# Kernel tuning notes

Measured on AMD Instinct MI355X. Metric: run time of the kernel, lower is better.

## Reference

```python
import jax, jax.numpy as jnp
import numpy as np

M, NQ, NKV = 8, 256, 4096
E, H, D = 1024, 16, 64  # embed_dim, num_heads, head_dim
SCALE = D ** -0.5


def setup_inputs() -> dict:
    key = jax.random.key(0)
    ks = jax.random.split(key, 6)
    zq = jax.random.normal(ks[0], (M, NQ, E), dtype=jnp.float32)
    zkv = jax.random.normal(ks[1], (M, NKV, E), dtype=jnp.float32)
    xq = jax.random.normal(ks[2], (M, NQ, E), dtype=jnp.float32)
    xkv = jax.random.normal(ks[3], (M, NKV, E), dtype=jnp.float32)
    Wq = jax.random.normal(ks[4], (E, H * D), dtype=jnp.float32) / np.sqrt(E)
    Wk = jax.random.normal(ks[5], (E, H * D), dtype=jnp.float32) / np.sqrt(E)
    raw_head_weights = jnp.ones((H,), dtype=jnp.float32)
    return {"zq": zq, "zkv": zkv, "xq": xq, "xkv": xkv,
            "Wq": Wq, "Wk": Wk, "raw_head_weights": raw_head_weights}


def reference(zq, zkv, xq, xkv, Wq, Wk, raw_head_weights):
    # project + split heads: [m, h, n, d]
    q = jnp.einsum('mne,ehd->mhnd', zq, Wq.reshape(E, H, D))
    k = jnp.einsum('mne,ehd->mhnd', zkv, Wk.reshape(E, H, D))
    # SDPA with V = xkv broadcast across heads
    scores = jnp.einsum('mhqd,mhkd->mhqk', q, k) * SCALE
    attn = jax.nn.softmax(scores, axis=-1)
    # attn @ V with broadcast V [m, nkv, dx] -> per-head outputs [m, h, nq, dx]
    out = jnp.einsum('mhqk,mkd->mhqd', attn, xkv)
    # head-weighted combine + residual
    head_weights = jax.nn.softmax(raw_head_weights, axis=0)
    xq_update = jnp.einsum('mhqd,h->mqd', out, head_weights)
    xq_out = xq + xq_update
    return (zq, xq_out)
```

## Files before the change

### kernel.cpp

```cpp
#include <hip/hip_runtime.h>
#include <hip/hip_bf16.h>
#include <stdint.h>

#define MB_  8
#define NQ_  256
#define NKV_ 4096
#define E_   1024
#define H_   16
#define D_   64

typedef __bf16 bf16x8 __attribute__((ext_vector_type(8)));
typedef float  f32x4  __attribute__((ext_vector_type(4)));
typedef unsigned short u16;
typedef unsigned short u16x8 __attribute__((ext_vector_type(8)));

#define MFMA16(a,b,c) __builtin_amdgcn_mfma_f32_16x16x32_bf16((a),(b),(c),0,0,0)

__device__ __forceinline__ u16 f2bf(float f) {
  uint32_t u = __float_as_uint(f);
  u += 0x7fffu + ((u >> 16) & 1u);
  return (u16)(u >> 16);
}

__device__ __forceinline__ void gload_lds16(const void* g, void* l) {
  __builtin_amdgcn_global_load_lds(
      (const __attribute__((address_space(1))) void*)g,
      (__attribute__((address_space(3))) void*)l, 16, 0, 0);
}

__device__ __forceinline__ void stage_tile(const char* __restrict__ g, int ldbytes,
                                           char* lds, int t) {
  int srcCB = (((t & 7) ^ ((t >> 3) & 7)) << 4);
  const char* gp = g + (long long)(t >> 3) * ldbytes + srcCB;
  char* lp = lds + ((t >> 6) << 10);
#pragma unroll
  for (int i = 0; i < 4; ++i) {
    gload_lds16(gp + (long long)(32 * i) * ldbytes, lp + i * 4096);
  }
}

__device__ __forceinline__ bf16x8 read_frag(const char* lds, int r, int cb) {
  return *(const bf16x8*)(lds + r * 128 + (cb ^ ((r & 7) << 4)));
}

template <int MODE>
__global__ __launch_bounds__(256, 2) void gemm_nt(
    const u16* __restrict__ A, const u16* __restrict__ Bt, void* __restrict__ Cv,
    int lda, int ldb, int ldc, int K,
    long long sA, long long sB, long long sC) {
  __shared__ __align__(16) char smA[16384];
  __shared__ __align__(16) char smB[16384];
  int zz = blockIdx.z;
  int b = (MODE == 2) ? (zz & 7) : zz;
  int ks = (MODE == 2) ? (zz >> 3) : 0;
  long long koff = (long long)ks * 1024;

  unsigned nwg = gridDim.x * gridDim.y;
  unsigned orig = blockIdx.y * gridDim.x + blockIdx.x;
  unsigned cpx = nwg >> 3;
  unsigned swz = (orig & 7) * cpx + (orig >> 3);
  unsigned bx = swz % gridDim.x, by = swz / gridDim.x;

  const char* Ap = (const char*)(A + (long long)b * sA + (long long)by * 128 * lda + koff);
  const char* Bp = (const char*)(Bt + (long long)b * sB + (long long)bx * 128 * ldb + koff);

  int t = threadIdx.x, lane = t & 63;
  int wm = t >> 7, wn = (t >> 6) & 1;
  int rl = lane & 15, kq = lane >> 4;

  f32x4 acc[4][4];
#pragma unroll
  for (int i = 0; i < 4; ++i)
#pragma unroll
    for (int j = 0; j < 4; ++j) acc[i][j] = (f32x4){0.f, 0.f, 0.f, 0.f};

  int ldab = lda * 2, ldbb = ldb * 2;
  for (int k0 = 0; k0 < K; k0 += 64) {
    stage_tile(Ap + k0 * 2, ldab, smA, t);
    stage_tile(Bp + k0 * 2, ldbb, smB, t);
    __syncthreads();
    bf16x8 af[4][2], bf[4][2];
#pragma unroll
    for (int f = 0; f < 4; ++f)
#pragma unroll
      for (int ksl = 0; ksl < 2; ++ksl) {
        af[f][ksl] = read_frag(smA, wm * 64 + f * 16 + rl, ksl * 64 + kq * 16);
        bf[f][ksl] = read_frag(smB, wn * 64 + f * 16 + rl, ksl * 64 + kq * 16);
      }
#pragma unroll
    for (int fm = 0; fm < 4; ++fm)
#pragma unroll
      for (int fn = 0; fn < 4; ++fn) {
        acc[fm][fn] = MFMA16(af[fm][0], bf[fn][0], acc[fm][fn]);
        acc[fm][fn] = MFMA16(af[fm][1], bf[fn][1], acc[fm][fn]);
      }
    __syncthreads();
  }

#pragma unroll
  for (int fm = 0; fm < 4; ++fm)
#pragma unroll
    for (int fn = 0; fn < 4; ++fn)
#pragma unroll
      for (int j = 0; j < 4; ++j) {
        int row = by * 128 + wm * 64 + fm * 16 + kq * 4 + j;
        int col = bx * 128 + wn * 64 + fn * 16 + rl;
        if (MODE == 0) {
          ((u16*)Cv)[(long long)b * sC + (long long)row * ldc + col] = f2bf(acc[fm][fn][j]);
        } else {
          ((float*)Cv)[((long long)(ks * 8 + b)) * sC + (long long)row * ldc + col] =
              acc[fm][fn][j];
        }
      }
}

__global__ void pv_combine_copy(const float* __restrict__ part, const float* __restrict__ xq,
                                const float* __restrict__ zq, float* __restrict__ out0,
                                float* __restrict__ out1) {
  int bid = blockIdx.x;
  if (bid < 2048) {
    int i = bid * 256 + threadIdx.x;
    ((float4*)out0)[i] = ((const float4*)zq)[i];
  } else {
    int i = (bid - 2048) * 256 + threadIdx.x;
    float4 s = ((const float4*)xq)[i];
#pragma unroll
    for (int k = 0; k < 4; ++k) {
      float4 p = ((const float4*)(part + (long long)k * 2097152))[i];
      s.x += p.x; s.y += p.y; s.z += p.z; s.w += p.w;
    }
    ((float4*)out1)[i] = s;
  }
}

__global__ __launch_bounds__(256, 4) void attn_stats(
    const u16* __restrict__ qg, const u16* __restrict__ kg,
    float* __restrict__ lstP) {
  __shared__ __align__(16) char smQ[16384];
  __shared__ __align__(16) char smK[16384];
  int kt = blockIdx.x, qt = blockIdx.y;
  int m = blockIdx.z >> 1, hh = blockIdx.z & 1;
  int t = threadIdx.x, lane = t & 63;
  int wm = t >> 7, wn = (t >> 6) & 1;
  int rl = lane & 15, kq = lane >> 4;

  const char* qbase = (const char*)(qg + ((long long)(m * NQ_ + qt * 128)) * 1024);
  const char* kbase = (const char*)(kg + ((long long)(m * NKV_ + kt * 128)) * 1024);

  for (int hi = 0; hi < 8; ++hi) {
    int h = hh * 8 + hi;
    stage_tile(qbase + h * 128, 2048, smQ, t);
    stage_tile(kbase + h * 128, 2048, smK, t);
    __syncthreads();
    bf16x8 kf[4][2], qf[4][2];
#pragma unroll
    for (int f = 0; f < 4; ++f)
#pragma unroll
      for (int ksl = 0; ksl < 2; ++ksl) {
        kf[f][ksl] = read_frag(smK, wm * 64 + f * 16 + rl, ksl * 64 + kq * 16);
        qf[f][ksl] = read_frag(smQ, wn * 64 + f * 16 + rl, ksl * 64 + kq * 16);
      }
    float rs[4] = {0.f, 0.f, 0.f, 0.f};
#pragma unroll
    for (int fm = 0; fm < 4; ++fm)
#pragma unroll
      for (int fn = 0; fn < 4; ++fn) {
        f32x4 sc = (f32x4){0.f, 0.f, 0.f, 0.f};
        sc = MFMA16(kf[fm][0], qf[fn][0], sc);
        sc = MFMA16(kf[fm][1], qf[fn][1], sc);
        rs[fn] += (__expf(sc[0]) + __expf(sc[1])) + (__expf(sc[2]) + __expf(sc[3]));
      }
#pragma unroll
    for (int fn = 0; fn < 4; ++fn) {
      float v = rs[fn];
      v += __shfl_xor(v, 16);
      v += __shfl_xor(v, 32);
      if (lane < 16) {
        int q = qt * 128 + wn * 64 + fn * 16 + rl;
        lstP[(long long)(kt * 2 + wm) * 32768 + ((m * H_ + h) << 8) + q] = v;
      }
    }
    __syncthreads();
  }
}

__global__ void stats_combine(const float* __restrict__ lp, float* __restrict__ lst) {
  int i = blockIdx.x * 256 + threadIdx.x;
  float s = 0.f;
#pragma unroll
  for (int k = 0; k < 64; ++k) s += lp[(long long)k * 32768 + i];
  lst[i] = s;
}

__global__ __launch_bounds__(256, 2) void pbar_kernel(
    const u16* __restrict__ qg, const u16* __restrict__ kg,
    const float* __restrict__ lstat,
    const float* __restrict__ rawhw, u16* __restrict__ Pbar) {
  __shared__ __align__(16) char smQ[16384];
  __shared__ __align__(16) char smK[16384];
  __shared__ float scf[2048];
  int kt = blockIdx.x, qt = blockIdx.y, m = blockIdx.z;
  int q0 = qt * 128, k0 = kt * 128;
  int t = threadIdx.x, lane = t & 63;
  int wm = t >> 7, wn = (t >> 6) & 1;
  int rl = lane & 15, kq = lane >> 4;

  float hm = -1e30f;
  for (int i = 0; i < H_; ++i) hm = fmaxf(hm, rawhw[i]);
  float hs = 0.f, hw[H_];
  for (int i = 0; i < H_; ++i) { hw[i] = __expf(rawhw[i] - hm); hs += hw[i]; }
  float hinv = 1.f / hs;
  for (int idx = t; idx < 2048; idx += 256) {
    int h = idx >> 7, r = idx & 127;
    scf[idx] = hw[h] * hinv / lstat[((m * H_ + h) << 8) + q0 + r];
  }

  f32x4 pacc[4][4];
#pragma unroll
  for (int i = 0; i < 4; ++i)
#pragma unroll
    for (int j = 0; j < 4; ++j) pacc[i][j] = (f32x4){0.f, 0.f, 0.f, 0.f};

  const char* qbase = (const char*)(qg + ((long long)(m * NQ_ + q0)) * 1024);
  const char* kbase = (const char*)(kg + ((long long)(m * NKV_ + k0)) * 1024);

  for (int h = 0; h < H_; ++h) {
    stage_tile(qbase + h * 128, 2048, smQ, t);
    stage_tile(kbase + h * 128, 2048, smK, t);
    __syncthreads();
    bf16x8 af[4][2], bfr[4][2];
#pragma unroll
    for (int f = 0; f < 4; ++f)
#pragma unroll
      for (int ksl = 0; ksl < 2; ++ksl) {
        af[f][ksl] = read_frag(smQ, wm * 64 + f * 16 + rl, ksl * 64 + kq * 16);
        bfr[f][ksl] = read_frag(smK, wn * 64 + f * 16 + rl, ksl * 64 + kq * 16);
      }
#pragma unroll
    for (int fm = 0; fm < 4; ++fm) {
      int rbase = wm * 64 + fm * 16 + kq * 4;
      float cf0 = scf[(h << 7) + rbase + 0];
      float cf1 = scf[(h << 7) + rbase + 1];
      float cf2 = scf[(h << 7) + rbase + 2];
      float cf3 = scf[(h << 7) + rbase + 3];
#pragma unroll
      for (int fn = 0; fn < 4; ++fn) {
        f32x4 sc = (f32x4){0.f, 0.f, 0.f, 0.f};
        sc = MFMA16(af[fm][0], bfr[fn][0], sc);
        sc = MFMA16(af[fm][1], bfr[fn][1], sc);
        pacc[fm][fn][0] += cf0 * __expf(sc[0]);
        pacc[fm][fn][1] += cf1 * __expf(sc[1]);
        pacc[fm][fn][2] += cf2 * __expf(sc[2]);
        pacc[fm][fn][3] += cf3 * __expf(sc[3]);
      }
    }
    __syncthreads();
  }
#pragma unroll
  for (int fm = 0; fm < 4; ++fm)
#pragma unroll
    for (int fn = 0; fn < 4; ++fn)
#pragma unroll
      for (int j = 0; j < 4; ++j) {
        int row = q0 + wm * 64 + fm * 16 + kq * 4 + j;
        int col = k0 + wn * 64 + fn * 16 + rl;
        Pbar[(((long long)m * NQ_ + row) << 12) + col] = f2bf(pacc[fm][fn][j]);
      }
}

__global__ void cvt8m(const float* __restrict__ zq, u16* __restrict__ zqb,
                      const float* __restrict__ zkv, u16* __restrict__ zkvb) {
  int bid = blockIdx.x;
  const float* in;
  u16* out;
  long long i;
  if (bid < 1024) { in = zq; out = zqb; i = (long long)bid * 256 + threadIdx.x; }
  else { in = zkv; out = zkvb; i = (long long)(bid - 1024) * 256 + threadIdx.x; }
  const float4* p = (const float4*)in + i * 2;
  float4 a = p[0], b = p[1];
  u16x8 v;
  v[0] = f2bf(a.x); v[1] = f2bf(a.y); v[2] = f2bf(a.z); v[3] = f2bf(a.w);
  v[4] = f2bf(b.x); v[5] = f2bf(b.y); v[6] = f2bf(b.z); v[7] = f2bf(b.w);
  *(u16x8*)(out + i * 8) = v;
}

__global__ void tcvt64(const float* __restrict__ in, u16* __restrict__ out,
                       int R, int C, long long sIn, long long sOut, float alpha) {
  __shared__ float tile[64][65];
  in += (long long)blockIdx.z * sIn;
  out += (long long)blockIdx.z * sOut;
  int r0 = blockIdx.x * 64, c0 = blockIdx.y * 64;
  int t = threadIdx.x;
  int rr = t >> 4, c4 = t & 15;
#pragma unroll
  for (int i = 0; i < 4; ++i) {
    float4 v = *(const float4*)(in + (long long)(r0 + rr + i * 16) * C + c0 + c4 * 4);
    float* d = &tile[rr + i * 16][c4 * 4];
    d[0] = v.x; d[1] = v.y; d[2] = v.z; d[3] = v.w;
  }
  __syncthreads();
  int cc = t >> 3, r8 = t & 7;
#pragma unroll
  for (int i = 0; i < 2; ++i) {
    int c = cc + i * 32;
    u16x8 v;
#pragma unroll
    for (int j = 0; j < 8; ++j) v[j] = f2bf(alpha * tile[r8 * 8 + j][c]);
    *(u16x8*)(out + (long long)(c0 + c) * R + r0 + r8 * 8) = v;
  }
}

extern "C" void kernel_launch(void* const* d_in, const int* in_sizes, int n_in,
                              void* d_out, int out_size, void* d_ws, size_t ws_size,
                              hipStream_t stream) {
  const float* zq  = (const float*)d_in[0];
  const float* zkv = (const float*)d_in[1];
  const float* xq  = (const float*)d_in[2];
  const float* xkv = (const float*)d_in[3];
  const float* Wq  = (const float*)d_in[4];
  const float* Wk  = (const float*)d_in[5];
  const float* rhw = (const float*)d_in[6];
  float* out = (float*)d_out;

  char* ws = (char*)d_ws;
  u16* WqT  = (u16*)(ws);
  u16* WkT  = (u16*)(ws + (2ull << 20));
  u16* zqb  = (u16*)(ws + (4ull << 20));
  u16* qb   = (u16*)(ws + (8ull << 20));
  u16* kb   = (u16*)(ws + (12ull << 20));
  u16* xkvT = (u16*)(ws + (76ull << 20));
  char* zr  = ws + (140ull << 20);
  u16* zkvb = (u16*)zr;
  u16* Pbar = (u16*)zr;
  float* lst  = (float*)(zr + (18ull << 20));
  float* lstP = (float*)(zr + (20ull << 20));
  float* pvP  = (float*)(zr + (28ull << 20));

  cvt8m<<<17408, 256, 0, stream>>>(zq, zqb, zkv, zkvb);
  tcvt64<<<dim3(16, 16, 1), 256, 0, stream>>>(Wq, WqT, 1024, 1024, 0, 0, 0.125f);
  tcvt64<<<dim3(16, 16, 1), 256, 0, stream>>>(Wk, WkT, 1024, 1024, 0, 0, 1.0f);
  tcvt64<<<dim3(64, 16, 8), 256, 0, stream>>>(xkv, xkvT, NKV_, E_,
                                              (long long)NKV_ * E_, (long long)NKV_ * E_, 1.0f);

  gemm_nt<0><<<dim3(8, 16, 1), 256, 0, stream>>>(zqb, WqT, qb,
                                                 1024, 1024, 1024, 1024, 0, 0, 0);
  gemm_nt<0><<<dim3(8, 256, 1), 256, 0, stream>>>(zkvb, WkT, kb,
                                                  1024, 1024, 1024, 1024, 0, 0, 0);

  attn_stats<<<dim3(32, 2, 16), 256, 0, stream>>>(qb, kb, lstP);
  stats_combine<<<128, 256, 0, stream>>>(lstP, lst);

  pbar_kernel<<<dim3(32, 2, 8), 256, 0, stream>>>(qb, kb, lst, rhw, Pbar);

  gemm_nt<2><<<dim3(8, 2, 32), 256, 0, stream>>>(Pbar, xkvT, pvP,
                                                 4096, 4096, 1024, 1024,
                                                 256LL * 4096, 1024LL * 4096,
                                                 256LL * 1024);
  pv_combine_copy<<<4096, 256, 0, stream>>>(pvP, xq, zq, out,
                                            out + (long long)MB_ * NQ_ * E_);
}
```

Baseline: 312.5 us.

## Add 256x256-tile pipelined GEMM for K projection and fuse prep conversion kernels

Replaces the 128x128 gemm_nt used for the large zkv@Wk projection with a new 512-thread kernel that uses 256x256 output tiles, a 4-deep LDS ring with XOR-swizzled async global-to-LDS loads, workgroup ID swizzling and s_setprio around the MFMA block. It also merges the four bf16 convert/transpose launches into one prep kernel that dispatches on block index. The larger tile is meant to raise arithmetic intensity, and the fused prep kernel cuts launch overhead. In exchange the GEMM needs 128KB of dynamic LDS and many accumulator registers, which lowers occupancy.

```diff
diff --git a/kernel.cpp b/kernel.cpp
--- a/kernel.cpp
+++ b/kernel.cpp
@@ -111,6 +111,96 @@
           ((float*)Cv)[((long long)(ks * 8 + b)) * sC + (long long)row * ldc + col] =
               acc[fm][fn][j];
         }
+      }
+}
+
+__device__ __forceinline__ void stage32(const char* __restrict__ g, int ldbytes,
+                                        char* ldsbuf, int t, long long koffB) {
+  int w = t >> 6, lane = t & 63;
+#pragma unroll
+  for (int i = 0; i < 2; ++i) {
+    int c = w + i * 8;
+    int slot = c * 64 + lane;
+    int row = slot >> 2, c16 = slot & 3;
+    int srcc = (c16 ^ ((row >> 1) & 3)) << 4;
+    gload_lds16(g + (long long)row * ldbytes + koffB + srcc,
+                ldsbuf + c * 1024);
+  }
+}
+
+__device__ __forceinline__ bf16x8 frag32(const char* ldsbuf, int r, int kq) {
+  return *(const bf16x8*)(ldsbuf + r * 64 + ((kq ^ ((r >> 1) & 3)) << 4));
+}
+
+__global__ __launch_bounds__(512, 2) void gemm256(
+    const u16* __restrict__ A, const u16* __restrict__ Bt, u16* __restrict__ C,
+    int lda, int ldb, int ldc, int K) {
+  extern __shared__ char lds[];
+
+  unsigned nwg = gridDim.x * gridDim.y;
+  unsigned orig = blockIdx.y * gridDim.x + blockIdx.x;
+  unsigned cpx = nwg >> 3;
+  unsigned swz = (orig & 7) * cpx + (orig >> 3);
+  unsigned bx = swz % gridDim.x, by = swz / gridDim.x;
+
+  const char* Ap = (const char*)(A + (long long)by * 256 * lda);
+  const char* Bp = (const char*)(Bt + (long long)bx * 256 * ldb);
+  int ldab = lda * 2, ldbb = ldb * 2;
+
+  int t = threadIdx.x, lane = t & 63;
+  int wid = t >> 6, wm = wid >> 2, wn = wid & 3;
+  int rl = lane & 15, kq = lane >> 4;
+
+  f32x4 acc[8][4];
+#pragma unroll
+  for (int i = 0; i < 8; ++i)
+#pragma unroll
+    for (int j = 0; j < 4; ++j) acc[i][j] = (f32x4){0.f, 0.f, 0.f, 0.f};
+
+  stage32(Ap, ldab, lds, t, 0);
+  stage32(Bp, ldbb, lds + 16384, t, 0);
+  stage32(Ap, ldab, lds + 32768, t, 64);
+  stage32(Bp, ldbb, lds + 32768 + 16384, t, 64);
+  asm volatile("s_waitcnt vmcnt(4)" ::: "memory");
+  asm volatile("s_barrier" ::: "memory");
+
+  int NT = K >> 5;
+  for (int ts = 0; ts < NT; ++ts) {
+    char* bufA = lds + (ts & 3) * 32768;
+    char* bufB = bufA + 16384;
+    if (ts + 2 < NT) {
+      char* nb = lds + ((ts + 2) & 3) * 32768;
+      stage32(Ap, ldab, nb, t, (long long)(ts + 2) << 6);
+      stage32(Bp, ldbb, nb + 16384, t, (long long)(ts + 2) << 6);
+    }
+    bf16x8 af[8], bv[4];
+#pragma unroll
+    for (int fr = 0; fr < 8; ++fr) af[fr] = frag32(bufA, wm * 128 + fr * 16 + rl, kq);
+#pragma unroll
+    for (int fc = 0; fc < 4; ++fc) bv[fc] = frag32(bufB, wn * 64 + fc * 16 + rl, kq);
+    __builtin_amdgcn_s_setprio(1);
+#pragma unroll
+    for (int fr = 0; fr < 8; ++fr)
+#pragma unroll
+      for (int fc = 0; fc < 4; ++fc)
+        acc[fr][fc] = MFMA16(af[fr], bv[fc], acc[fr][fc]);
+    __builtin_amdgcn_s_setprio(0);
+    if (ts + 2 < NT)
+      asm volatile("s_waitcnt vmcnt(4)" ::: "memory");
+    else
+      asm volatile("s_waitcnt vmcnt(0)" ::: "memory");
+    asm volatile("s_barrier" ::: "memory");
+  }
+
+#pragma unroll
+  for (int fr = 0; fr < 8; ++fr)
+#pragma unroll
+    for (int fc = 0; fc < 4; ++fc)
+#pragma unroll
+      for (int j = 0; j < 4; ++j) {
+        int row = by * 256 + wm * 128 + fr * 16 + kq * 4 + j;
+        int col = bx * 256 + wn * 64 + fc * 16 + rl;
+        C[(long long)row * ldc + col] = f2bf(acc[fr][fc][j]);
       }
 }
 
@@ -268,28 +358,42 @@
       }
 }
 
-__global__ void cvt8m(const float* __restrict__ zq, u16* __restrict__ zqb,
-                      const float* __restrict__ zkv, u16* __restrict__ zkvb) {
+__global__ void prep_kernel(const float* __restrict__ zq, u16* __restrict__ zqb,
+                            const float* __restrict__ zkv, u16* __restrict__ zkvb,
+                            const float* __restrict__ Wq, u16* __restrict__ WqT,
+                            const float* __restrict__ Wk, u16* __restrict__ WkT,
+                            const float* __restrict__ xkv, u16* __restrict__ xkvT) {
+  __shared__ float tile[64][65];
   int bid = blockIdx.x;
-  const float* in;
-  u16* out;
-  long long i;
-  if (bid < 1024) { in = zq; out = zqb; i = (long long)bid * 256 + threadIdx.x; }
-  else { in = zkv; out = zkvb; i = (long long)(bid - 1024) * 256 + threadIdx.x; }
-  const float4* p = (const float4*)in + i * 2;
-  float4 a = p[0], b = p[1];
-  u16x8 v;
-  v[0] = f2bf(a.x); v[1] = f2bf(a.y); v[2] = f2bf(a.z); v[3] = f2bf(a.w);
-  v[4] = f2bf(b.x); v[5] = f2bf(b.y); v[6] = f2bf(b.z); v[7] = f2bf(b.w);
-  *(u16x8*)(out + i * 8) = v;
-}
-
-__global__ void tcvt64(const float* __restrict__ in, u16* __restrict__ out,
-                       int R, int C, long long sIn, long long sOut, float alpha) {
-  __shared__ float tile[64][65];
-  in += (long long)blockIdx.z * sIn;
-  out += (long long)blockIdx.z * sOut;
-  int r0 = blockIdx.x * 64, c0 = blockIdx.y * 64;
+  if (bid < 17408) {
+    const float* in; u16* out; long long i;
+    if (bid < 1024) { in = zq; out = zqb; i = (long long)bid * 256 + threadIdx.x; }
+    else { in = zkv; out = zkvb; i = (long long)(bid - 1024) * 256 + threadIdx.x; }
+    const float4* p = (const float4*)in + i * 2;
+    float4 a = p[0], b = p[1];
+    u16x8 v;
+    v[0] = f2bf(a.x); v[1] = f2bf(a.y); v[2] = f2bf(a.z); v[3] = f2bf(a.w);
+    v[4] = f2bf(b.x); v[5] = f2bf(b.y); v[6] = f2bf(b.z); v[7] = f2bf(b.w);
+    *(u16x8*)(out + i * 8) = v;
+    return;
+  }
+  const float* in; u16* out; int R, C; float alpha; int r0, c0;
+  if (bid < 17664) {
+    int id = bid - 17408;
+    in = Wq; out = WqT; R = 1024; C = 1024; alpha = 0.125f;
+    r0 = (id & 15) * 64; c0 = (id >> 4) * 64;
+  } else if (bid < 17920) {
+    int id = bid - 17664;
+    in = Wk; out = WkT; R = 1024; C = 1024; alpha = 1.0f;
+    r0 = (id & 15) * 64; c0 = (id >> 4) * 64;
+  } else {
+    int id = bid - 17920;
+    int bz = id >> 10, rem = id & 1023;
+    in = xkv + (long long)bz * NKV_ * E_;
+    out = xkvT + (long long)bz * NKV_ * E_;
+    R = NKV_; C = E_; alpha = 1.0f;
+    r0 = (rem & 63) * 64; c0 = (rem >> 6) * 64;
+  }
   int t = threadIdx.x;
   int rr = t >> 4, c4 = t & 15;
 #pragma unroll
@@ -336,16 +440,14 @@
   float* lstP = (float*)(zr + (20ull << 20));
   float* pvP  = (float*)(zr + (28ull << 20));
 
-  cvt8m<<<17408, 256, 0, stream>>>(zq, zqb, zkv, zkvb);
-  tcvt64<<<dim3(16, 16, 1), 256, 0, stream>>>(Wq, WqT, 1024, 1024, 0, 0, 0.125f);
-  tcvt64<<<dim3(16, 16, 1), 256, 0, stream>>>(Wk, WkT, 1024, 1024, 0, 0, 1.0f);
-  tcvt64<<<dim3(64, 16, 8), 256, 0, stream>>>(xkv, xkvT, NKV_, E_,
-                                              (long long)NKV_ * E_, (long long)NKV_ * E_, 1.0f);
+  (void)hipFuncSetAttribute((const void*)gemm256,
+                            hipFuncAttributeMaxDynamicSharedMemorySize, 131072);
+
+  prep_kernel<<<26112, 256, 0, stream>>>(zq, zqb, zkv, zkvb, Wq, WqT, Wk, WkT, xkv, xkvT);
 
   gemm_nt<0><<<dim3(8, 16, 1), 256, 0, stream>>>(zqb, WqT, qb,
                                                  1024, 1024, 1024, 1024, 0, 0, 0);
-  gemm_nt<0><<<dim3(8, 256, 1), 256, 0, stream>>>(zkvb, WkT, kb,
-                                                  1024, 1024, 1024, 1024, 0, 0, 0);
+  gemm256<<<dim3(4, 128, 1), 512, 131072, stream>>>(zkvb, WkT, kb, 1024, 1024, 1024, 1024);
 
   attn_stats<<<dim3(32, 2, 16), 256, 0, stream>>>(qb, kb, lstP);
   stats_combine<<<128, 256, 0, stream>>>(lstP, lst);
```

Result: faster. 300.9 us (-3.7%).
